# Kernel optimization log

Measured on AMD Instinct MI355X. Metric: run time of the kernel, lower is better.

The kernel has to match this reference:

```python
import jax, jax.numpy as jnp
import numpy as np

N = 50000  # num nodes


def _gcn_layer(x, W, b, src, dst, dinv):
    # PyG GCNConv: transform first, then normalized neighbor aggregation
    h = x @ W                                   # [N, out]
    norm = dinv[src] * dinv[dst]                # [E]
    msg = h[src] * norm[:, None]                # gather + scale, [E, out]
    agg = jax.ops.segment_sum(msg, dst, num_segments=N)
    agg = agg + h * (dinv * dinv)[:, None]      # self-loop term (weight 1)
    return agg + b


def setup_inputs() -> dict:
    key = jax.random.key(0)
    ks = jax.random.split(key, 9)
    x = jax.random.normal(ks[0], (N, 256), dtype=jnp.float32)
    edge_index = jax.random.randint(ks[1], (2, 800000), 0, N, dtype=jnp.int64)
    def lin(kw, kb, fan_in, fan_out):
        s = 1.0 / np.sqrt(fan_in)
        W = jax.random.uniform(kw, (fan_in, fan_out), jnp.float32, -s, s)
        b = jax.random.uniform(kb, (fan_out,), jnp.float32, -s, s)
        return W, b
    W0, b0 = lin(ks[2], ks[3], 256, 128)
    W1, b1 = lin(ks[4], ks[5], 128, 128)
    W2, b2 = lin(ks[6], ks[7], 128, 64)
    return {"x": x, "edge_index": edge_index,
            "W0": W0, "b0": b0, "W1": W1, "b1": b1, "W2": W2, "b2": b2}


def reference(x, edge_index, W0, b0, W1, b1, W2, b2):
    src, dst = edge_index[0], edge_index[1]
    # degree with implicit self loops (edge weights = 1)
    deg = jax.ops.segment_sum(jnp.ones_like(dst, dtype=x.dtype), dst,
                              num_segments=N) + 1.0
    dinv = jax.lax.rsqrt(deg)
    h = jax.nn.relu(_gcn_layer(x, W0, b0, src, dst, dinv))
    h = jax.nn.relu(_gcn_layer(h, W1, b1, src, dst, dinv))
    out = _gcn_layer(h, W2, b2, src, dst, dinv)  # no relu on final layer
    return out
```

## Files before the change

kernel.cpp:

```cpp
#include <hip/hip_runtime.h>

#define NNODES 50000
#define NEDGES 800000
#define CHUNK 3125

typedef __attribute__((ext_vector_type(8))) short short8;
typedef __attribute__((ext_vector_type(4))) float floatx4;
typedef __attribute__((ext_vector_type(8))) _Float16 f16x8;

__device__ __forceinline__ void async16(const void* g, void* l) {
    __builtin_amdgcn_global_load_lds(
        (const __attribute__((address_space(1))) unsigned int*)g,
        (__attribute__((address_space(3))) unsigned int*)l, 16, 0, 0);
}

__device__ __forceinline__ void split_bf16(float v, short& hi, short& lo) {
    unsigned u = __float_as_uint(v);
    unsigned hu = u & 0xffff0000u;
    hi = (short)(hu >> 16);
    float r = v - __uint_as_float(hu);
    lo = (short)(__float_as_uint(r) >> 16);
}


#define PREP_WBLK 224
#define PREP_TOT  (PREP_WBLK + 256)

__global__ __launch_bounds__(256) void k_prep(
    const float* __restrict__ W0, short* __restrict__ W0h, short* __restrict__ W0l,
    const float* __restrict__ W1, short* __restrict__ W1h, short* __restrict__ W1l,
    const float* __restrict__ W2, short* __restrict__ W2h, short* __restrict__ W2l,
    const int* __restrict__ dst, int* __restrict__ hist2d) {
    int b = blockIdx.x, t = threadIdx.x;
    if (b < PREP_WBLK) {
        int id = b * 256 + t;
        const float* W; short *Wh, *Wl; int K, F;
        if (id < 32768) { W = W0; Wh = W0h; Wl = W0l; K = 256; F = 128; }
        else if (id < 49152) { id -= 32768; W = W1; Wh = W1h; Wl = W1l; K = 128; F = 128; }
        else if (id < 57344) { id -= 49152; W = W2; Wh = W2h; Wl = W2l; K = 128; F = 64; }
        else return;
        int f = id / K, k = id - f * K;
        short h, l;
        split_bf16(W[(size_t)k * F + f], h, l);
        Wh[id] = h;
        Wl[id] = l;
    } else {
        __shared__ int h[256];
        int bb = b - PREP_WBLK;
        h[t] = 0;
        __syncthreads();
        int e0 = bb * CHUNK;
#pragma unroll
        for (int k = 0; k < 13; k++) {
            int o = k * 256 + t;
            if (o < CHUNK) atomicAdd(&h[dst[e0 + o] >> 8], 1);
        }
        __syncthreads();
        hist2d[bb * 256 + t] = h[t];
    }
}


__global__ __launch_bounds__(256) void k_scan(const int* __restrict__ hist2d,
                                              int* __restrict__ scanned,
                                              int* __restrict__ gbase) {
    int t = threadIdx.x;
    int run = 0;
    for (int bb = 0; bb < 256; bb++) {
        int v = hist2d[bb * 256 + t];
        scanned[bb * 256 + t] = run;
        run += v;
    }
    __shared__ int ex[256];
    ex[t] = run;
    __syncthreads();
    for (int o = 1; o < 256; o <<= 1) {
        int xx = (t >= o) ? ex[t - o] : 0;
        __syncthreads();
        ex[t] += xx;
        __syncthreads();
    }
    gbase[t] = ex[t] - run;
    if (t == 255) gbase[256] = ex[t];
}

__global__ __launch_bounds__(256) void k_p2(const int* __restrict__ src,
                                            const int* __restrict__ dst,
                                            const int* __restrict__ scanned,
                                            const int* __restrict__ gbase,
                                            unsigned* __restrict__ buck) {
    __shared__ int cur[256];
    int t = threadIdx.x, b = blockIdx.x;
    cur[t] = gbase[t] + scanned[b * 256 + t];
    __syncthreads();
    int e0 = b * CHUNK;
#pragma unroll
    for (int k = 0; k < 13; k++) {
        int o = k * 256 + t;
        if (o < CHUNK) {
            int s = src[e0 + o], d = dst[e0 + o];
            int p = atomicAdd(&cur[d >> 8], 1);
            buck[p] = (unsigned)s | ((unsigned)(d & 255) << 16);
        }
    }
}

__global__ __launch_bounds__(256) void k_p3(const unsigned* __restrict__ buck,
                                            const int* __restrict__ gbase,
                                            int* __restrict__ rowptr,
                                            float* __restrict__ dinv,
                                            int* __restrict__ ssrc) {
    __shared__ int ex[256], cur[256], h[256];
    int t = threadIdx.x, b = blockIdx.x;
    int s0 = gbase[b];
    int S = gbase[b + 1] - s0;
    h[t] = 0;
    __syncthreads();
    for (int i = t; i < S; i += 256)
        atomicAdd(&h[(buck[s0 + i] >> 16) & 255], 1);
    __syncthreads();
    int v = h[t];
    ex[t] = v;
    __syncthreads();
    for (int o = 1; o < 256; o <<= 1) {
        int xx = (t >= o) ? ex[t - o] : 0;
        __syncthreads();
        ex[t] += xx;
        __syncthreads();
    }
    int excl = ex[t] - v;
    int n = b * 256 + t;
    if (n < NNODES) {
        rowptr[n] = s0 + excl;
        dinv[n] = rsqrtf((float)v + 1.0f);
    }
    if (b == 0 && t == 0) rowptr[NNODES] = NEDGES;
    cur[t] = excl;
    __syncthreads();
    for (int i = t; i < S; i += 256) {
        unsigned pk = buck[s0 + i];
        int dl = (pk >> 16) & 255;
        int p = atomicAdd(&cur[dl], 1);
        ssrc[s0 + p] = (int)(pk & 0xFFFFu);
    }
}


__global__ __launch_bounds__(256) void k_gemm0(
    const float* __restrict__ x, const short* __restrict__ Bh,
    const short* __restrict__ Bl, const float* __restrict__ dinv,
    _Float16* __restrict__ g16) {
    __shared__ __align__(16) short sAh[64 * 64], sAl[64 * 64];
    __shared__ __align__(16) short sBh[128 * 64], sBl[128 * 64];
    const int t = threadIdx.x, lane = t & 63, w = t >> 6;
    const int row0 = blockIdx.x * 64;
    const int lr = lane >> 3, lz = lane & 7;
    const int swz = (lz ^ lr) * 8;
    const int fr = lane & 15, fq = lane >> 4;
    floatx4 acc[8] = {};
    const int ar = t >> 2, ac = t & 3;
    int garow = row0 + ar;
    if (garow >= NNODES) garow = NNODES - 1;
    const float* xrow = x + (size_t)garow * 256 + ac * 16;

    for (int k0 = 0; k0 < 256; k0 += 64) {
        const float4* xp = (const float4*)(xrow + k0);
        float4 f0 = xp[0], f1 = xp[1], f2 = xp[2], f3 = xp[3];
        float va[16] = {f0.x, f0.y, f0.z, f0.w, f1.x, f1.y, f1.z, f1.w,
                        f2.x, f2.y, f2.z, f2.w, f3.x, f3.y, f3.z, f3.w};
        short8 h0, h1, l0, l1;
#pragma unroll
        for (int j = 0; j < 8; j++) {
            short h, l;
            split_bf16(va[j], h, l);     h0[j] = h; l0[j] = l;
            split_bf16(va[8 + j], h, l); h1[j] = h; l1[j] = l;
        }
        int c0 = ac * 2;
        *(short8*)&sAh[ar * 64 + ((c0 ^ (ar & 7)) * 8)] = h0;
        *(short8*)&sAh[ar * 64 + (((c0 + 1) ^ (ar & 7)) * 8)] = h1;
        *(short8*)&sAl[ar * 64 + ((c0 ^ (ar & 7)) * 8)] = l0;
        *(short8*)&sAl[ar * 64 + (((c0 + 1) ^ (ar & 7)) * 8)] = l1;
#pragma unroll
        for (int jj = 0; jj < 4; jj++) {
            int j = w * 4 + jj;
            size_t go = (size_t)(j * 8 + lr) * 256 + k0 + swz;
            async16(&Bh[go], &sBh[j * 512 + lane * 8]);
            async16(&Bl[go], &sBl[j * 512 + lane * 8]);
        }
        __syncthreads();
#pragma unroll
        for (int ks = 0; ks < 2; ks++) {
            int R = w * 16 + fr;
            int ca = ((ks * 4 + fq) ^ (R & 7)) * 8;
            short8 ah = *(const short8*)&sAh[R * 64 + ca];
            short8 al = *(const short8*)&sAl[R * 64 + ca];
#pragma unroll
            for (int nt = 0; nt < 8; nt++) {
                int n = nt * 16 + fr;
                int cb = ((ks * 4 + fq) ^ (n & 7)) * 8;
                short8 bh = *(const short8*)&sBh[n * 64 + cb];
                short8 bl = *(const short8*)&sBl[n * 64 + cb];
                acc[nt] = __builtin_amdgcn_mfma_f32_16x16x32_bf16(ah, bh, acc[nt], 0, 0, 0);
                acc[nt] = __builtin_amdgcn_mfma_f32_16x16x32_bf16(ah, bl, acc[nt], 0, 0, 0);
                acc[nt] = __builtin_amdgcn_mfma_f32_16x16x32_bf16(al, bh, acc[nt], 0, 0, 0);
            }
        }
        __syncthreads();
    }
#pragma unroll
    for (int rr = 0; rr < 4; rr++) {
        int gw = row0 + w * 16 + fq * 4 + rr;
        if (gw < NNODES) {
            float dv = dinv[gw];
#pragma unroll
            for (int nt = 0; nt < 8; nt++)
                g16[(size_t)gw * 128 + nt * 16 + fr] =
                    (_Float16)(acc[nt][rr] * dv);
        }
    }
}


template <int BN>
__global__ __launch_bounds__(256) void k_fagg(
    const _Float16* __restrict__ gin,
    const int* __restrict__ ssrc,
    const int* __restrict__ rowptr,
    const float* __restrict__ dinv,
    const float* __restrict__ bias,
    const short* __restrict__ Bh, const short* __restrict__ Bl,
    _Float16* __restrict__ gout) {
    constexpr int BM = 32;
    constexpr int NT = BN / 32;
    __shared__ __align__(16) short sAh[2 * BM * 64], sAl[2 * BM * 64];
    __shared__ __align__(16) char uB[16384];

    const int t = threadIdx.x, lane = t & 63, w = t >> 6;
    const int row0 = blockIdx.x * BM;

    int (*sED)[64] = (int(*)[64])uB;
    const int ln = t >> 3;
    const int c8 = t & 7;
    const f16x8* gp = (const f16x8*)gin;

    int gr = row0 + ln;
    if (gr >= NNODES) gr = NNODES - 1;
    int e0 = rowptr[gr], e1 = rowptr[gr + 1];
    int deg = e1 - e0;
    int cnt = deg < 64 ? deg : 64;
    for (int i = c8; i < cnt; i += 8) sED[ln][i] = ssrc[e0 + i];
    __syncthreads();

    f16x8 svA = gp[(size_t)gr * 16 + c8];
    f16x8 svB = gp[(size_t)gr * 16 + c8 + 8];
    float aA0[8], aA1[8], aB0[8], aB1[8];
#pragma unroll
    for (int j = 0; j < 8; j++) {
        aA0[j] = (float)svA[j]; aA1[j] = 0.f;
        aB0[j] = (float)svB[j]; aB1[j] = 0.f;
    }
    int i = 0;
    for (; i + 4 <= cnt; i += 4) {
        int s0 = sED[ln][i],     s1 = sED[ln][i + 1];
        int s2 = sED[ln][i + 2], s3 = sED[ln][i + 3];
        f16x8 vA0 = gp[(size_t)s0 * 16 + c8];
        f16x8 vB0 = gp[(size_t)s0 * 16 + c8 + 8];
        f16x8 vA1 = gp[(size_t)s1 * 16 + c8];
        f16x8 vB1 = gp[(size_t)s1 * 16 + c8 + 8];
        f16x8 vA2 = gp[(size_t)s2 * 16 + c8];
        f16x8 vB2 = gp[(size_t)s2 * 16 + c8 + 8];
        f16x8 vA3 = gp[(size_t)s3 * 16 + c8];
        f16x8 vB3 = gp[(size_t)s3 * 16 + c8 + 8];
#pragma unroll
        for (int j = 0; j < 8; j++) {
            aA0[j] += (float)vA0[j] + (float)vA2[j];
            aA1[j] += (float)vA1[j] + (float)vA3[j];
            aB0[j] += (float)vB0[j] + (float)vB2[j];
            aB1[j] += (float)vB1[j] + (float)vB3[j];
        }
    }
    for (; i < cnt; i++) {
        int s = sED[ln][i];
        f16x8 vA = gp[(size_t)s * 16 + c8];
        f16x8 vB = gp[(size_t)s * 16 + c8 + 8];
#pragma unroll
        for (int j = 0; j < 8; j++) {
            aA0[j] += (float)vA[j];
            aB0[j] += (float)vB[j];
        }
    }
    for (int e = e0 + 64; e < e1; e++) {
        int s = ssrc[e];
        f16x8 vA = gp[(size_t)s * 16 + c8];
        f16x8 vB = gp[(size_t)s * 16 + c8 + 8];
#pragma unroll
        for (int j = 0; j < 8; j++) {
            aA0[j] += (float)vA[j];
            aB0[j] += (float)vB[j];
        }
    }

    {
        float dv = dinv[gr];
        short8 h8, l8;
#pragma unroll
        for (int j = 0; j < 8; j++) {
            float o = (aA0[j] + aA1[j]) * dv + bias[c8 * 8 + j];
            o = fmaxf(o, 0.f);
            short h, l;
            split_bf16(o, h, l);
            h8[j] = h; l8[j] = l;
        }
        int ao0 = ln * 64 + ((c8 ^ (ln & 7)) * 8);
        *(short8*)&sAh[ao0] = h8;
        *(short8*)&sAl[ao0] = l8;
#pragma unroll
        for (int j = 0; j < 8; j++) {
            float o = (aB0[j] + aB1[j]) * dv + bias[(c8 + 8) * 8 + j];
            o = fmaxf(o, 0.f);
            short h, l;
            split_bf16(o, h, l);
            h8[j] = h; l8[j] = l;
        }
        int ao1 = BM * 64 + ao0;
        *(short8*)&sAh[ao1] = h8;
        *(short8*)&sAl[ao1] = l8;
    }
    __syncthreads();

    const int fr = lane & 15, fq = lane >> 4;
    const int lr = lane >> 3, lz = lane & 7;
    const int swz = (lz ^ lr) * 8;
    const int wr = w >> 1, wc = w & 1;
    floatx4 acc[NT] = {};

    if constexpr (BN == 128) {
        short* sB = (short*)uB;
#pragma unroll
        for (int kt = 0; kt < 2; kt++) {
#pragma unroll
            for (int jj = 0; jj < 4; jj++) {
                int j = w * 4 + jj;
                size_t go = (size_t)(j * 8 + lr) * 128 + kt * 64 + swz;
                async16(&Bh[go], &sB[j * 512 + lane * 8]);
            }
            __syncthreads();
#pragma unroll
            for (int ks = 0; ks < 2; ks++) {
                int R = wr * 16 + fr;
                int ca = kt * (BM * 64) + R * 64 + (((ks * 4 + fq) ^ (R & 7)) * 8);
                short8 ah = *(const short8*)&sAh[ca];
                short8 al = *(const short8*)&sAl[ca];
#pragma unroll
                for (int nt = 0; nt < NT; nt++) {
                    int n = wc * (BN / 2) + nt * 16 + fr;
                    int cb = n * 64 + (((ks * 4 + fq) ^ (n & 7)) * 8);
                    short8 bh = *(const short8*)&sB[cb];
                    acc[nt] = __builtin_amdgcn_mfma_f32_16x16x32_bf16(ah, bh, acc[nt], 0, 0, 0);
                    acc[nt] = __builtin_amdgcn_mfma_f32_16x16x32_bf16(al, bh, acc[nt], 0, 0, 0);
                }
            }
            __syncthreads();
#pragma unroll
            for (int jj = 0; jj < 4; jj++) {
                int j = w * 4 + jj;
                size_t go = (size_t)(j * 8 + lr) * 128 + kt * 64 + swz;
                async16(&Bl[go], &sB[j * 512 + lane * 8]);
            }
            __syncthreads();
#pragma unroll
            for (int ks = 0; ks < 2; ks++) {
                int R = wr * 16 + fr;
                int ca = kt * (BM * 64) + R * 64 + (((ks * 4 + fq) ^ (R & 7)) * 8);
                short8 ah = *(const short8*)&sAh[ca];
#pragma unroll
                for (int nt = 0; nt < NT; nt++) {
                    int n = wc * (BN / 2) + nt * 16 + fr;
                    int cb = n * 64 + (((ks * 4 + fq) ^ (n & 7)) * 8);
                    short8 bl = *(const short8*)&sB[cb];
                    acc[nt] = __builtin_amdgcn_mfma_f32_16x16x32_bf16(ah, bl, acc[nt], 0, 0, 0);
                }
            }
            __syncthreads();
        }
    } else {
        short* sBh_ = (short*)uB;
        short* sBl_ = (short*)uB + 64 * 64;
#pragma unroll
        for (int kt = 0; kt < 2; kt++) {
#pragma unroll
            for (int jj = 0; jj < 2; jj++) {
                int j = w * 2 + jj;
                size_t go = (size_t)(j * 8 + lr) * 128 + kt * 64 + swz;
                async16(&Bh[go], &sBh_[j * 512 + lane * 8]);
                async16(&Bl[go], &sBl_[j * 512 + lane * 8]);
            }
            __syncthreads();
#pragma unroll
            for (int ks = 0; ks < 2; ks++) {
                int R = wr * 16 + fr;
                int ca = kt * (BM * 64) + R * 64 + (((ks * 4 + fq) ^ (R & 7)) * 8);
                short8 ah = *(const short8*)&sAh[ca];
                short8 al = *(const short8*)&sAl[ca];
#pragma unroll
                for (int nt = 0; nt < NT; nt++) {
                    int n = wc * (BN / 2) + nt * 16 + fr;
                    int cb = n * 64 + (((ks * 4 + fq) ^ (n & 7)) * 8);
                    short8 bh = *(const short8*)&sBh_[cb];
                    short8 bl = *(const short8*)&sBl_[cb];
                    acc[nt] = __builtin_amdgcn_mfma_f32_16x16x32_bf16(ah, bh, acc[nt], 0, 0, 0);
                    acc[nt] = __builtin_amdgcn_mfma_f32_16x16x32_bf16(ah, bl, acc[nt], 0, 0, 0);
                    acc[nt] = __builtin_amdgcn_mfma_f32_16x16x32_bf16(al, bh, acc[nt], 0, 0, 0);
                }
            }
            __syncthreads();
        }
    }

#pragma unroll
    for (int rr = 0; rr < 4; rr++) {
        int grow = row0 + wr * 16 + fq * 4 + rr;
        if (grow < NNODES) {
            float dv = dinv[grow];
#pragma unroll
            for (int nt = 0; nt < NT; nt++)
                gout[(size_t)grow * BN + wc * (BN / 2) + nt * 16 + fr] =
                    (_Float16)(acc[nt][rr] * dv);
        }
    }
}


__global__ __launch_bounds__(256) void k_agg64(const _Float16* __restrict__ g,
                                               const int* __restrict__ ssrc,
                                               const int* __restrict__ rowptr,
                                               const float* __restrict__ dinv,
                                               const float* __restrict__ bias,
                                               float* __restrict__ outf) {
    constexpr int NPB = 64;
    __shared__ int sED[NPB][64];
    int t = threadIdx.x;
    int ln = t >> 2;
    int c8 = t & 3;
    int n = blockIdx.x * NPB + ln;
    bool valid = (n < NNODES);
    int nc = valid ? n : NNODES - 1;

    int e0 = rowptr[nc], e1 = rowptr[nc + 1];
    int deg = e1 - e0;
    int cnt = deg < 64 ? deg : 64;
    for (int i = c8; i < cnt; i += 4) sED[ln][i] = ssrc[e0 + i];
    __syncthreads();

    const f16x8* gp = (const f16x8*)g;
    f16x8 svA = gp[(size_t)nc * 8 + c8];
    f16x8 svB = gp[(size_t)nc * 8 + c8 + 4];
    float aA0[8], aA1[8], aB0[8], aB1[8];
#pragma unroll
    for (int j = 0; j < 8; j++) {
        aA0[j] = (float)svA[j]; aA1[j] = 0.f;
        aB0[j] = (float)svB[j]; aB1[j] = 0.f;
    }
    int i = 0;
    for (; i + 4 <= cnt; i += 4) {
        int s0 = sED[ln][i],     s1 = sED[ln][i + 1];
        int s2 = sED[ln][i + 2], s3 = sED[ln][i + 3];
        f16x8 vA0 = gp[(size_t)s0 * 8 + c8];
        f16x8 vB0 = gp[(size_t)s0 * 8 + c8 + 4];
        f16x8 vA1 = gp[(size_t)s1 * 8 + c8];
        f16x8 vB1 = gp[(size_t)s1 * 8 + c8 + 4];
        f16x8 vA2 = gp[(size_t)s2 * 8 + c8];
        f16x8 vB2 = gp[(size_t)s2 * 8 + c8 + 4];
        f16x8 vA3 = gp[(size_t)s3 * 8 + c8];
        f16x8 vB3 = gp[(size_t)s3 * 8 + c8 + 4];
#pragma unroll
        for (int j = 0; j < 8; j++) {
            aA0[j] += (float)vA0[j] + (float)vA2[j];
            aA1[j] += (float)vA1[j] + (float)vA3[j];
            aB0[j] += (float)vB0[j] + (float)vB2[j];
            aB1[j] += (float)vB1[j] + (float)vB3[j];
        }
    }
    for (; i < cnt; i++) {
        int s = sED[ln][i];
        f16x8 vA = gp[(size_t)s * 8 + c8];
        f16x8 vB = gp[(size_t)s * 8 + c8 + 4];
#pragma unroll
        for (int j = 0; j < 8; j++) {
            aA0[j] += (float)vA[j];
            aB0[j] += (float)vB[j];
        }
    }
    for (int e = e0 + 64; e < e1; e++) {
        int s = ssrc[e];
        f16x8 vA = gp[(size_t)s * 8 + c8];
        f16x8 vB = gp[(size_t)s * 8 + c8 + 4];
#pragma unroll
        for (int j = 0; j < 8; j++) {
            aA0[j] += (float)vA[j];
            aB0[j] += (float)vB[j];
        }
    }

    if (!valid) return;
    float dv = dinv[nc];
    float oA[8], oB[8];
#pragma unroll
    for (int j = 0; j < 8; j++) {
        oA[j] = (aA0[j] + aA1[j]) * dv + bias[c8 * 8 + j];
        oB[j] = (aB0[j] + aB1[j]) * dv + bias[(c8 + 4) * 8 + j];
    }
    *(float4*)&outf[(size_t)n * 64 + c8 * 8] =
        make_float4(oA[0], oA[1], oA[2], oA[3]);
    *(float4*)&outf[(size_t)n * 64 + c8 * 8 + 4] =
        make_float4(oA[4], oA[5], oA[6], oA[7]);
    *(float4*)&outf[(size_t)n * 64 + (c8 + 4) * 8] =
        make_float4(oB[0], oB[1], oB[2], oB[3]);
    *(float4*)&outf[(size_t)n * 64 + (c8 + 4) * 8 + 4] =
        make_float4(oB[4], oB[5], oB[6], oB[7]);
}


static inline size_t align256(size_t x) { return (x + 255) & ~(size_t)255; }

extern "C" void kernel_launch(void* const* d_in, const int* in_sizes, int n_in,
                              void* d_out, int out_size, void* d_ws, size_t ws_size,
                              hipStream_t stream) {
    const float* x  = (const float*)d_in[0];
    const int*   ei = (const int*)d_in[1];
    const float* W0 = (const float*)d_in[2];
    const float* b0 = (const float*)d_in[3];
    const float* W1 = (const float*)d_in[4];
    const float* b1 = (const float*)d_in[5];
    const float* W2 = (const float*)d_in[6];
    const float* b2 = (const float*)d_in[7];
    float* out = (float*)d_out;

    const int* src = ei;
    const int* dst = ei + NEDGES;

    char* w = (char*)d_ws;
    size_t off = 0;
    float* dinv    = (float*)(w + off); off = align256(off + NNODES * 4);
    int* rowptr    = (int*)(w + off);   off = align256(off + (NNODES + 1) * 4);
    int* hist2d    = (int*)(w + off);   off = align256(off + 256 * 256 * 4);
    int* scanned   = (int*)(w + off);   off = align256(off + 256 * 256 * 4);
    int* gbase     = (int*)(w + off);   off = align256(off + 257 * 4);
    unsigned* buck = (unsigned*)(w + off); off = align256(off + (size_t)NEDGES * 4);
    int* ssrc      = (int*)(w + off);   off = align256(off + (size_t)NEDGES * 4);
    short* W0h     = (short*)(w + off); off = align256(off + 256 * 128 * 2);
    short* W0l     = (short*)(w + off); off = align256(off + 256 * 128 * 2);
    short* W1h     = (short*)(w + off); off = align256(off + 128 * 128 * 2);
    short* W1l     = (short*)(w + off); off = align256(off + 128 * 128 * 2);
    short* W2h     = (short*)(w + off); off = align256(off + 128 * 64 * 2);
    short* W2l     = (short*)(w + off); off = align256(off + 128 * 64 * 2);
    _Float16* g16a = (_Float16*)(w + off); off = align256(off + (size_t)NNODES * 128 * 2);
    _Float16* g16b = (_Float16*)(w + off); off = align256(off + (size_t)NNODES * 128 * 2);
    _Float16* g16c = (_Float16*)(w + off); off = align256(off + (size_t)NNODES * 64 * 2);

    const int MB = (NNODES + 63) / 64;
    const int FB = (NNODES + 31) / 32;
    const int AB = (NNODES + 63) / 64;

    k_prep<<<PREP_TOT, 256, 0, stream>>>(W0, W0h, W0l, W1, W1h, W1l,
                                         W2, W2h, W2l, dst, hist2d);
    k_scan<<<1, 256, 0, stream>>>(hist2d, scanned, gbase);
    k_p2<<<256, 256, 0, stream>>>(src, dst, scanned, gbase, buck);
    k_p3<<<256, 256, 0, stream>>>(buck, gbase, rowptr, dinv, ssrc);

    k_gemm0<<<MB, 256, 0, stream>>>(x, W0h, W0l, dinv, g16a);
    k_fagg<128><<<FB, 256, 0, stream>>>(g16a, ssrc, rowptr, dinv, b0,
                                        W1h, W1l, g16b);
    k_fagg<64><<<FB, 256, 0, stream>>>(g16b, ssrc, rowptr, dinv, b1,
                                       W2h, W2l, g16c);
    k_agg64<<<AB, 256, 0, stream>>>(g16c, ssrc, rowptr, dinv, b2, out);
    (void)in_sizes; (void)n_in; (void)out_size; (void)ws_size;
}
```

Measured before the change: 231.3 us.

## Fuse layer-0 GEMM into bucket-scatter kernel and defer dinv scaling to aggregation

The first-layer GEMM no longer depends on dinv, so it is merged into the edge bucket-scatter kernel as extra blocks and runs concurrently with graph preprocessing instead of after CSR construction. To make this possible, the source-side dinv scaling moves into the first aggregation kernel, which loads dinv per neighbor into shared memory and multiplies each gathered row by it. This removes a launch and a serialization point, at the cost of extra per-edge dinv loads and multiplies in layer-1 aggregation and of shared-memory-heavy GEMM blocks co-scheduled with the scatter blocks.

```diff
diff --git a/kernel.cpp b/kernel.cpp
--- a/kernel.cpp
+++ b/kernel.cpp
@@ -84,23 +84,99 @@
     if (t == 255) gbase[256] = ex[t];
 }
 
-__global__ __launch_bounds__(256) void k_p2(const int* __restrict__ src,
-                                            const int* __restrict__ dst,
-                                            const int* __restrict__ scanned,
-                                            const int* __restrict__ gbase,
-                                            unsigned* __restrict__ buck) {
-    __shared__ int cur[256];
-    int t = threadIdx.x, b = blockIdx.x;
-    cur[t] = gbase[t] + scanned[b * 256 + t];
-    __syncthreads();
-    int e0 = b * CHUNK;
-#pragma unroll
-    for (int k = 0; k < 13; k++) {
-        int o = k * 256 + t;
-        if (o < CHUNK) {
-            int s = src[e0 + o], d = dst[e0 + o];
-            int p = atomicAdd(&cur[d >> 8], 1);
-            buck[p] = (unsigned)s | ((unsigned)(d & 255) << 16);
+
+#define G0_MB ((NNODES + 63) / 64)
+
+__global__ __launch_bounds__(256) void k_p2g0(
+    const int* __restrict__ src, const int* __restrict__ dst,
+    const int* __restrict__ scanned, const int* __restrict__ gbase,
+    unsigned* __restrict__ buck,
+    const float* __restrict__ x, const short* __restrict__ Bh,
+    const short* __restrict__ Bl, _Float16* __restrict__ g16) {
+    __shared__ __align__(16) short sAh[64 * 64], sAl[64 * 64];
+    __shared__ __align__(16) short sBh[128 * 64], sBl[128 * 64];
+
+    if (blockIdx.x < 256) {
+        int* cur = (int*)sAh;
+        int t = threadIdx.x, b = blockIdx.x;
+        cur[t] = gbase[t] + scanned[b * 256 + t];
+        __syncthreads();
+        int e0 = b * CHUNK;
+#pragma unroll
+        for (int k = 0; k < 13; k++) {
+            int o = k * 256 + t;
+            if (o < CHUNK) {
+                int s = src[e0 + o], d = dst[e0 + o];
+                int p = atomicAdd(&cur[d >> 8], 1);
+                buck[p] = (unsigned)s | ((unsigned)(d & 255) << 16);
+            }
+        }
+        return;
+    }
+
+    const int t = threadIdx.x, lane = t & 63, w = t >> 6;
+    const int row0 = (blockIdx.x - 256) * 64;
+    const int lr = lane >> 3, lz = lane & 7;
+    const int swz = (lz ^ lr) * 8;
+    const int fr = lane & 15, fq = lane >> 4;
+    floatx4 acc[8] = {};
+    const int ar = t >> 2, ac = t & 3;
+    int garow = row0 + ar;
+    if (garow >= NNODES) garow = NNODES - 1;
+    const float* xrow = x + (size_t)garow * 256 + ac * 16;
+
+    for (int k0 = 0; k0 < 256; k0 += 64) {
+        const float4* xp = (const float4*)(xrow + k0);
+        float4 f0 = xp[0], f1 = xp[1], f2 = xp[2], f3 = xp[3];
+        float va[16] = {f0.x, f0.y, f0.z, f0.w, f1.x, f1.y, f1.z, f1.w,
+                        f2.x, f2.y, f2.z, f2.w, f3.x, f3.y, f3.z, f3.w};
+        short8 h0, h1, l0, l1;
+#pragma unroll
+        for (int j = 0; j < 8; j++) {
+            short h, l;
+            split_bf16(va[j], h, l);     h0[j] = h; l0[j] = l;
+            split_bf16(va[8 + j], h, l); h1[j] = h; l1[j] = l;
+        }
+        int c0 = ac * 2;
+        *(short8*)&sAh[ar * 64 + ((c0 ^ (ar & 7)) * 8)] = h0;
+        *(short8*)&sAh[ar * 64 + (((c0 + 1) ^ (ar & 7)) * 8)] = h1;
+        *(short8*)&sAl[ar * 64 + ((c0 ^ (ar & 7)) * 8)] = l0;
+        *(short8*)&sAl[ar * 64 + (((c0 + 1) ^ (ar & 7)) * 8)] = l1;
+#pragma unroll
+        for (int jj = 0; jj < 4; jj++) {
+            int j = w * 4 + jj;
+            size_t go = (size_t)(j * 8 + lr) * 256 + k0 + swz;
+            async16(&Bh[go], &sBh[j * 512 + lane * 8]);
+            async16(&Bl[go], &sBl[j * 512 + lane * 8]);
+        }
+        __syncthreads();
+#pragma unroll
+        for (int ks = 0; ks < 2; ks++) {
+            int R = w * 16 + fr;
+            int ca = ((ks * 4 + fq) ^ (R & 7)) * 8;
+            short8 ah = *(const short8*)&sAh[R * 64 + ca];
+            short8 al = *(const short8*)&sAl[R * 64 + ca];
+#pragma unroll
+            for (int nt = 0; nt < 8; nt++) {
+                int n = nt * 16 + fr;
+                int cb = ((ks * 4 + fq) ^ (n & 7)) * 8;
+                short8 bh = *(const short8*)&sBh[n * 64 + cb];
+                short8 bl = *(const short8*)&sBl[n * 64 + cb];
+                acc[nt] = __builtin_amdgcn_mfma_f32_16x16x32_bf16(ah, bh, acc[nt], 0, 0, 0);
+                acc[nt] = __builtin_amdgcn_mfma_f32_16x16x32_bf16(ah, bl, acc[nt], 0, 0, 0);
+                acc[nt] = __builtin_amdgcn_mfma_f32_16x16x32_bf16(al, bh, acc[nt], 0, 0, 0);
+            }
+        }
+        __syncthreads();
+    }
+#pragma unroll
+    for (int rr = 0; rr < 4; rr++) {
+        int gw = row0 + w * 16 + fq * 4 + rr;
+        if (gw < NNODES) {
+#pragma unroll
+            for (int nt = 0; nt < 8; nt++)
+                g16[(size_t)gw * 128 + nt * 16 + fr] =
+                    (_Float16)(acc[nt][rr]);
         }
     }
 }
@@ -146,82 +222,7 @@
 }
 
 
-__global__ __launch_bounds__(256) void k_gemm0(
-    const float* __restrict__ x, const short* __restrict__ Bh,
-    const short* __restrict__ Bl, const float* __restrict__ dinv,
-    _Float16* __restrict__ g16) {
-    __shared__ __align__(16) short sAh[64 * 64], sAl[64 * 64];
-    __shared__ __align__(16) short sBh[128 * 64], sBl[128 * 64];
-    const int t = threadIdx.x, lane = t & 63, w = t >> 6;
-    const int row0 = blockIdx.x * 64;
-    const int lr = lane >> 3, lz = lane & 7;
-    const int swz = (lz ^ lr) * 8;
-    const int fr = lane & 15, fq = lane >> 4;
-    floatx4 acc[8] = {};
-    const int ar = t >> 2, ac = t & 3;
-    int garow = row0 + ar;
-    if (garow >= NNODES) garow = NNODES - 1;
-    const float* xrow = x + (size_t)garow * 256 + ac * 16;
-
-    for (int k0 = 0; k0 < 256; k0 += 64) {
-        const float4* xp = (const float4*)(xrow + k0);
-        float4 f0 = xp[0], f1 = xp[1], f2 = xp[2], f3 = xp[3];
-        float va[16] = {f0.x, f0.y, f0.z, f0.w, f1.x, f1.y, f1.z, f1.w,
-                        f2.x, f2.y, f2.z, f2.w, f3.x, f3.y, f3.z, f3.w};
-        short8 h0, h1, l0, l1;
-#pragma unroll
-        for (int j = 0; j < 8; j++) {
-            short h, l;
-            split_bf16(va[j], h, l);     h0[j] = h; l0[j] = l;
-            split_bf16(va[8 + j], h, l); h1[j] = h; l1[j] = l;
-        }
-        int c0 = ac * 2;
-        *(short8*)&sAh[ar * 64 + ((c0 ^ (ar & 7)) * 8)] = h0;
-        *(short8*)&sAh[ar * 64 + (((c0 + 1) ^ (ar & 7)) * 8)] = h1;
-        *(short8*)&sAl[ar * 64 + ((c0 ^ (ar & 7)) * 8)] = l0;
-        *(short8*)&sAl[ar * 64 + (((c0 + 1) ^ (ar & 7)) * 8)] = l1;
-#pragma unroll
-        for (int jj = 0; jj < 4; jj++) {
-            int j = w * 4 + jj;
-            size_t go = (size_t)(j * 8 + lr) * 256 + k0 + swz;
-            async16(&Bh[go], &sBh[j * 512 + lane * 8]);
-            async16(&Bl[go], &sBl[j * 512 + lane * 8]);
-        }
-        __syncthreads();
-#pragma unroll
-        for (int ks = 0; ks < 2; ks++) {
-            int R = w * 16 + fr;
-            int ca = ((ks * 4 + fq) ^ (R & 7)) * 8;
-            short8 ah = *(const short8*)&sAh[R * 64 + ca];
-            short8 al = *(const short8*)&sAl[R * 64 + ca];
-#pragma unroll
-            for (int nt = 0; nt < 8; nt++) {
-                int n = nt * 16 + fr;
-                int cb = ((ks * 4 + fq) ^ (n & 7)) * 8;
-                short8 bh = *(const short8*)&sBh[n * 64 + cb];
-                short8 bl = *(const short8*)&sBl[n * 64 + cb];
-                acc[nt] = __builtin_amdgcn_mfma_f32_16x16x32_bf16(ah, bh, acc[nt], 0, 0, 0);
-                acc[nt] = __builtin_amdgcn_mfma_f32_16x16x32_bf16(ah, bl, acc[nt], 0, 0, 0);
-                acc[nt] = __builtin_amdgcn_mfma_f32_16x16x32_bf16(al, bh, acc[nt], 0, 0, 0);
-            }
-        }
-        __syncthreads();
-    }
-#pragma unroll
-    for (int rr = 0; rr < 4; rr++) {
-        int gw = row0 + w * 16 + fq * 4 + rr;
-        if (gw < NNODES) {
-            float dv = dinv[gw];
-#pragma unroll
-            for (int nt = 0; nt < 8; nt++)
-                g16[(size_t)gw * 128 + nt * 16 + fr] =
-                    (_Float16)(acc[nt][rr] * dv);
-        }
-    }
-}
-
-
-template <int BN>
+template <int BN, bool SIN>
 __global__ __launch_bounds__(256) void k_fagg(
     const _Float16* __restrict__ gin,
     const int* __restrict__ ssrc,
@@ -239,6 +240,7 @@
     const int row0 = blockIdx.x * BM;
 
     int (*sED)[64] = (int(*)[64])uB;
+    float (*sDV)[64] = (float(*)[64])(uB + 8192);
     const int ln = t >> 3;
     const int c8 = t & 7;
     const f16x8* gp = (const f16x8*)gin;
@@ -248,16 +250,26 @@
     int e0 = rowptr[gr], e1 = rowptr[gr + 1];
     int deg = e1 - e0;
     int cnt = deg < 64 ? deg : 64;
-    for (int i = c8; i < cnt; i += 8) sED[ln][i] = ssrc[e0 + i];
-    __syncthreads();
-
+    if constexpr (SIN) {
+        for (int i = c8; i < cnt; i += 8) sED[ln][i] = ssrc[e0 + i];
+    } else {
+        for (int i = c8; i < cnt; i += 8) {
+            int s = ssrc[e0 + i];
+            sED[ln][i] = s;
+            sDV[ln][i] = dinv[s];
+        }
+    }
+    __syncthreads();
+
+    float dvn = dinv[gr];
     f16x8 svA = gp[(size_t)gr * 16 + c8];
     f16x8 svB = gp[(size_t)gr * 16 + c8 + 8];
+    const float sw = SIN ? 1.0f : dvn;
     float aA0[8], aA1[8], aB0[8], aB1[8];
 #pragma unroll
     for (int j = 0; j < 8; j++) {
-        aA0[j] = (float)svA[j]; aA1[j] = 0.f;
-        aB0[j] = (float)svB[j]; aB1[j] = 0.f;
+        aA0[j] = (float)svA[j] * sw; aA1[j] = 0.f;
+        aB0[j] = (float)svB[j] * sw; aB1[j] = 0.f;
     }
     int i = 0;
     for (; i + 4 <= cnt; i += 4) {
@@ -271,41 +283,54 @@
         f16x8 vB2 = gp[(size_t)s2 * 16 + c8 + 8];
         f16x8 vA3 = gp[(size_t)s3 * 16 + c8];
         f16x8 vB3 = gp[(size_t)s3 * 16 + c8 + 8];
-#pragma unroll
-        for (int j = 0; j < 8; j++) {
-            aA0[j] += (float)vA0[j] + (float)vA2[j];
-            aA1[j] += (float)vA1[j] + (float)vA3[j];
-            aB0[j] += (float)vB0[j] + (float)vB2[j];
-            aB1[j] += (float)vB1[j] + (float)vB3[j];
+        if constexpr (SIN) {
+#pragma unroll
+            for (int j = 0; j < 8; j++) {
+                aA0[j] += (float)vA0[j] + (float)vA2[j];
+                aA1[j] += (float)vA1[j] + (float)vA3[j];
+                aB0[j] += (float)vB0[j] + (float)vB2[j];
+                aB1[j] += (float)vB1[j] + (float)vB3[j];
+            }
+        } else {
+            float w0 = sDV[ln][i],     w1 = sDV[ln][i + 1];
+            float w2 = sDV[ln][i + 2], w3 = sDV[ln][i + 3];
+#pragma unroll
+            for (int j = 0; j < 8; j++) {
+                aA0[j] += (float)vA0[j] * w0 + (float)vA2[j] * w2;
+                aA1[j] += (float)vA1[j] * w1 + (float)vA3[j] * w3;
+                aB0[j] += (float)vB0[j] * w0 + (float)vB2[j] * w2;
+                aB1[j] += (float)vB1[j] * w1 + (float)vB3[j] * w3;
+            }
         }
     }
     for (; i < cnt; i++) {
         int s = sED[ln][i];
+        float ws = SIN ? 1.0f : sDV[ln][i];
         f16x8 vA = gp[(size_t)s * 16 + c8];
         f16x8 vB = gp[(size_t)s * 16 + c8 + 8];
 #pragma unroll
         for (int j = 0; j < 8; j++) {
-            aA0[j] += (float)vA[j];
-            aB0[j] += (float)vB[j];
+            aA0[j] += (float)vA[j] * ws;
+            aB0[j] += (float)vB[j] * ws;
         }
     }
     for (int e = e0 + 64; e < e1; e++) {
         int s = ssrc[e];
+        float ws = SIN ? 1.0f : dinv[s];
         f16x8 vA = gp[(size_t)s * 16 + c8];
         f16x8 vB = gp[(size_t)s * 16 + c8 + 8];
 #pragma unroll
         for (int j = 0; j < 8; j++) {
-            aA0[j] += (float)vA[j];
-            aB0[j] += (float)vB[j];
+            aA0[j] += (float)vA[j] * ws;
+            aB0[j] += (float)vB[j] * ws;
         }
     }
 
     {
-        float dv = dinv[gr];
         short8 h8, l8;
 #pragma unroll
         for (int j = 0; j < 8; j++) {
-            float o = (aA0[j] + aA1[j]) * dv + bias[c8 * 8 + j];
+            float o = (aA0[j] + aA1[j]) * dvn + bias[c8 * 8 + j];
             o = fmaxf(o, 0.f);
             short h, l;
             split_bf16(o, h, l);
@@ -316,7 +341,7 @@
         *(short8*)&sAl[ao0] = l8;
 #pragma unroll
         for (int j = 0; j < 8; j++) {
-            float o = (aB0[j] + aB1[j]) * dv + bias[(c8 + 8) * 8 + j];
+            float o = (aB0[j] + aB1[j]) * dvn + bias[(c8 + 8) * 8 + j];
             o = fmaxf(o, 0.f);
             short h, l;
             split_bf16(o, h, l);
@@ -558,21 +583,20 @@
     _Float16* g16b = (_Float16*)(w + off); off = align256(off + (size_t)NNODES * 128 * 2);
     _Float16* g16c = (_Float16*)(w + off); off = align256(off + (size_t)NNODES * 64 * 2);
 
-    const int MB = (NNODES + 63) / 64;
     const int FB = (NNODES + 31) / 32;
     const int AB = (NNODES + 63) / 64;
 
     k_prep<<<PREP_TOT, 256, 0, stream>>>(W0, W0h, W0l, W1, W1h, W1l,
                                          W2, W2h, W2l, dst, hist2d);
     k_scan<<<1, 256, 0, stream>>>(hist2d, scanned, gbase);
-    k_p2<<<256, 256, 0, stream>>>(src, dst, scanned, gbase, buck);
+    k_p2g0<<<256 + G0_MB, 256, 0, stream>>>(src, dst, scanned, gbase, buck,
+                                            x, W0h, W0l, g16a);
     k_p3<<<256, 256, 0, stream>>>(buck, gbase, rowptr, dinv, ssrc);
 
-    k_gemm0<<<MB, 256, 0, stream>>>(x, W0h, W0l, dinv, g16a);
-    k_fagg<128><<<FB, 256, 0, stream>>>(g16a, ssrc, rowptr, dinv, b0,
-                                        W1h, W1l, g16b);
-    k_fagg<64><<<FB, 256, 0, stream>>>(g16b, ssrc, rowptr, dinv, b1,
-                                       W2h, W2l, g16c);
+    k_fagg<128, false><<<FB, 256, 0, stream>>>(g16a, ssrc, rowptr, dinv, b0,
+                                               W1h, W1l, g16b);
+    k_fagg<64, true><<<FB, 256, 0, stream>>>(g16b, ssrc, rowptr, dinv, b1,
+                                             W2h, W2l, g16c);
     k_agg64<<<AB, 256, 0, stream>>>(g16c, ssrc, rowptr, dinv, b2, out);
     (void)in_sizes; (void)n_in; (void)out_size; (void)ws_size;
 }
```

After: 235.9 us. About the same (+2.0%).
